# Kernel tuning notes

Hardware: AMD Instinct MI355X
Metric: run time of the kernel (lower is better)

## Reference

```python
import jax, jax.numpy as jnp
import numpy as np

B, G, C = 8, 512, 32  # batch, grid size, channel width (INIT_DIM)
NPB = 32768           # nonzeros per batch element


def _sconv(x, k, stride, pad):
    # dense conv; sparse semantics recovered by masking with the output
    # coordinate occupancy (Minkowski conv only produces active outputs)
    return jax.lax.conv_general_dilated(
        x, k, (stride, stride), [(pad, pad), (pad, pad)],
        dimension_numbers=('NHWC', 'HWIO', 'NHWC'))


def _downsample_mask(m):
    # ME strided output coord exists iff any input coord in the 2x2 cell is active
    return jax.lax.reduce_window(m, 0.0, jax.lax.max, (1, 2, 2, 1), (1, 2, 2, 1), 'VALID')


def setup_inputs() -> dict:
    key = jax.random.key(0)
    ks = jax.random.split(key, 16)
    b = jnp.repeat(jnp.arange(B, dtype=jnp.int32), NPB)
    yx = jax.random.randint(ks[0], (B * NPB, 2), 0, G, dtype=jnp.int32)
    coords = jnp.concatenate([b[:, None], yx], axis=1)          # [N,3] (b,y,x)
    feats = jax.random.normal(ks[1], (B * NPB, 1), jnp.float32)  # 1 feature/nnz
    x2 = jax.random.normal(ks[2], (B, 3), jnp.float32)
    # Minkowski conv kernels (bias=False by default); HWIO layout
    K1 = jax.random.normal(ks[3], (5, 5, 1, C), jnp.float32) * 0.28   # kaiming-ish
    K2 = jax.random.normal(ks[4], (3, 3, C, C), jnp.float32) * 0.083
    K3 = jax.random.normal(ks[5], (3, 3, C, C), jnp.float32) * 0.083
    K4 = jax.random.normal(ks[6], (3, 3, C, C), jnp.float32) * 0.083
    # feature MLP: Linear(3,64) -> ReLU -> Linear(64,32)
    W1 = jax.random.normal(ks[7], (3, 64), jnp.float32) * 0.3
    b1 = jnp.zeros((64,), jnp.float32)
    W2 = jax.random.normal(ks[8], (64, 32), jnp.float32) * 0.25
    b2 = jnp.zeros((32,), jnp.float32)
    # matrix_embedding: Linear(64,128) -> ReLU
    W3 = jax.random.normal(ks[9], (64, 128), jnp.float32) * 0.18
    b3 = jnp.zeros((128,), jnp.float32)
    return {'coords': coords, 'feats': feats, 'x2': x2,
            'K1': K1, 'K2': K2, 'K3': K3, 'K4': K4,
            'W1': W1, 'b1': b1, 'W2': W2, 'b2': b2, 'W3': W3, 'b3': b3}


def reference(coords, feats, x2, K1, K2, K3, K4, W1, b1, W2, b2, W3, b3):
    bi, yi, xi = coords[:, 0], coords[:, 1], coords[:, 2]
    grid = jnp.zeros((B, G, G, 1), jnp.float32).at[bi, yi, xi, 0].set(feats[:, 0])
    m1 = jnp.zeros((B, G, G, 1), jnp.float32).at[bi, yi, xi, 0].set(1.0)
    # layer1: k=5 s=1 (output coords == input coords)
    y1 = jax.nn.relu(_sconv(grid, K1, 1, 2)) * m1
    # layers 2-4: k=3 s=2; centered at even positions, masked by strided occupancy
    m2 = _downsample_mask(m1)
    y2 = jax.nn.relu(_sconv(y1, K2, 2, 1)) * m2
    m3 = _downsample_mask(m2)
    y3 = jax.nn.relu(_sconv(y2, K3, 2, 1)) * m3
    m4 = _downsample_mask(m3)
    y4 = jax.nn.relu(_sconv(y3, K4, 2, 1)) * m4
    # global average pool over active output coordinates per batch
    cnt = jnp.sum(m4, axis=(1, 2))                      # [B,1]
    pooled = jnp.sum(y4, axis=(1, 2)) / jnp.maximum(cnt, 1.0)  # [B,32]
    # aux feature MLP
    h = jax.nn.relu(x2[:, :3] @ W1 + b1) @ W2 + b2      # [B,32]
    z = jnp.concatenate([pooled, h], axis=1)            # [B,64]
    return jax.nn.relu(z @ W3 + b3)                     # [B,128]
```

## Files before the change

kernel.cpp:

```cpp
#include <hip/hip_runtime.h>
#include <hip/hip_bf16.h>
#include <stdint.h>


static constexpr int G_ = 512;
static constexpr int NPTS = 8 * 32768;

#define DEVI __device__ __forceinline__

typedef __attribute__((ext_vector_type(8))) short bf16x8;
typedef __attribute__((ext_vector_type(4))) float f32x4;
typedef __attribute__((ext_vector_type(4))) unsigned u32x4;

DEVI float bf_lo(unsigned w) { return __uint_as_float(w << 16); }
DEVI float bf_hi(unsigned w) { return __uint_as_float(w & 0xFFFF0000u); }
DEVI unsigned comp(const uint4& v, int i) {
  return i == 0 ? v.x : i == 1 ? v.y : i == 2 ? v.z : v.w;
}
DEVI unsigned short f2bf_bits(float f) {
  unsigned u = __float_as_uint(f);
  unsigned r = u + 0x7FFFu + ((u >> 16) & 1u);
  return (unsigned short)(r >> 16);
}
DEVI unsigned pack2(float a, float b) {
  return (unsigned)f2bf_bits(a) | ((unsigned)f2bf_bits(b) << 16);
}

__global__ __launch_bounds__(256) void k_scatter(const int* __restrict__ coords,
                                                 int* __restrict__ idxg) {
  int i = blockIdx.x * 256 + threadIdx.x;
  if (i >= NPTS) return;
  int b = coords[3 * i], y = coords[3 * i + 1], x = coords[3 * i + 2];
  atomicMax(&idxg[((size_t)b * G_ + y) * G_ + x], i);
}

__global__ __launch_bounds__(256) void k_grid(const int* __restrict__ idxg,
                                              const float* __restrict__ feats,
                                              unsigned* __restrict__ grid2) {
  int i = blockIdx.x * 256 + threadIdx.x;
  int v = idxg[i];
  float f = (v >= 0) ? feats[v] : 0.0f;
  unsigned short hb = f2bf_bits(f);
  unsigned short lb = f2bf_bits(f - __uint_as_float((unsigned)hb << 16));
  grid2[i] = (unsigned)hb | ((unsigned)lb << 16);
}

__global__ __launch_bounds__(256) void k_packw(
    const float* __restrict__ K1f, const float* __restrict__ K2,
    const float* __restrict__ K3, const float* __restrict__ K4,
    unsigned short* __restrict__ pw1h, unsigned short* __restrict__ pw1l,
    unsigned short* __restrict__ pw2, unsigned short* __restrict__ pw3,
    unsigned short* __restrict__ pw4) {
  const int t = threadIdx.x;
  if (t < 128) {
    int h = t >> 6, ln = t & 63;
    int g2 = ln >> 4, co = 2 * (ln & 15) + h;
#pragma unroll
    for (int j = 0; j < 8; j++) {
      int k = 8 * g2 + j;
      float v = (k < 25) ? K1f[k * 32 + co] : 0.f;
      unsigned short hb = f2bf_bits(v);
      pw1h[t * 8 + j] = hb;
      pw1l[t * 8 + j] = f2bf_bits(v - __uint_as_float((unsigned)hb << 16));
    }
  }
  const float* Ks[3] = {K2, K3, K4};
  unsigned short* ps[3] = {pw2, pw3, pw4};
  for (int m = 0; m < 3; m++)
    for (int e = t; e < 1152; e += 256) {
      int kk = e >> 7, rem = e & 127;
      int h = rem >> 6, ln = rem & 63;
      int g2 = ln >> 4, co = 2 * (ln & 15) + h;
#pragma unroll
      for (int j = 0; j < 8; j++)
        ps[m][e * 8 + j] = f2bf_bits(Ks[m][((kk * 32) + 8 * g2 + j) * 32 + co]);
    }
}

__global__ __launch_bounds__(256) void k_masks(const int* __restrict__ idxg,
                                               float* __restrict__ m2,
                                               float* __restrict__ m3,
                                               float* __restrict__ m4) {
  __shared__ float sm2[32][32];
  __shared__ float sm3[16][16];
  const int b = blockIdx.z, ty0 = blockIdx.y * 32, tx0 = blockIdx.x * 32;
  const int t = threadIdx.x;
  for (int i = t; i < 1024; i += 256) {
    int r = i >> 5, c = i & 31;
    const int* p = idxg + ((size_t)b * 512 + 2 * (ty0 + r)) * 512 + 2 * (tx0 + c);
    float v = ((p[0] & p[1] & p[512] & p[513]) >= 0) ? 1.f : 0.f;
    m2[((size_t)b * 256 + ty0 + r) * 256 + tx0 + c] = v;
    sm2[r][c] = v;
  }
  __syncthreads();
  {
    int r = t >> 4, c = t & 15;
    float v = fmaxf(fmaxf(sm2[2 * r][2 * c], sm2[2 * r][2 * c + 1]),
                    fmaxf(sm2[2 * r + 1][2 * c], sm2[2 * r + 1][2 * c + 1]));
    m3[((size_t)b * 128 + (ty0 >> 1) + r) * 128 + (tx0 >> 1) + c] = v;
    sm3[r][c] = v;
  }
  __syncthreads();
  if (t < 64) {
    int r = t >> 3, c = t & 7;
    float v = fmaxf(fmaxf(sm3[2 * r][2 * c], sm3[2 * r][2 * c + 1]),
                    fmaxf(sm3[2 * r + 1][2 * c], sm3[2 * r + 1][2 * c + 1]));
    m4[((size_t)b * 64 + (ty0 >> 2) + r) * 64 + (tx0 >> 2) + c] = v;
  }
}

__global__ __launch_bounds__(256, 3) void k_conv12(
    const unsigned* __restrict__ grid2, const int* __restrict__ idxg,
    const unsigned short* __restrict__ pw1h,
    const unsigned short* __restrict__ pw1l,
    const unsigned short* __restrict__ pw2, const float* __restrict__ m2,
    __hip_bfloat16* __restrict__ y2) {
  __shared__ unsigned s_grid[21 * 40];
  __shared__ unsigned short s_m1[17 * 34];
  __shared__ unsigned short s_y1[17 * 33 * 32];

  const int t = threadIdx.x;
  const int b = blockIdx.z, by = blockIdx.y, bx = blockIdx.x;
  const int gyb = 16 * by - 3, gxb = 32 * bx - 3;
  const size_t ibase = (size_t)b * G_ * G_;

  for (int i = t; i < 21 * 37; i += 256) {
    int rr = i / 37, cc = i - rr * 37;
    int gy = gyb + rr, gx = gxb + cc;
    unsigned v = 0;
    if (gy >= 0 && gy < G_ && gx >= 0 && gx < G_)
      v = grid2[ibase + (size_t)gy * G_ + gx];
    s_grid[rr * 40 + cc] = v;
  }
  for (int i = t; i < 17 * 33; i += 256) {
    int rr = i / 33, cc = i - rr * 33;
    int gy = gyb + 2 + rr, gx = gxb + 2 + cc;
    unsigned short mv = 0;
    if (gy >= 0 && gy < G_ && gx >= 0 && gx < G_)
      mv = (idxg[ibase + (size_t)gy * G_ + gx] >= 0) ? 1 : 0;
    s_m1[rr * 34 + cc] = mv;
  }

  const int lane = t & 63, w = t >> 6;
  const int r = lane & 15, g = lane >> 4;

  bf16x8 b1h[2], b1l[2];
#pragma unroll
  for (int h = 0; h < 2; h++) {
    b1h[h] = *(const bf16x8*)&pw1h[(h * 64 + lane) * 8];
    b1l[h] = *(const bf16x8*)&pw1l[(h * 64 + lane) * 8];
  }
  bf16x8 bw2[9][2];
#pragma unroll
  for (int kk = 0; kk < 9; kk++)
#pragma unroll
    for (int h = 0; h < 2; h++)
      bw2[kk][h] = *(const bf16x8*)&pw2[((kk * 2 + h) * 64 + lane) * 8];

  int reloff[8]; bool tval[8];
#pragma unroll
  for (int j = 0; j < 8; j++) {
    int k = 8 * g + j;
    tval[j] = (k < 25);
    int kq = tval[j] ? k : 0;
    reloff[j] = (kq / 5) * 40 + (kq % 5);
  }

  __syncthreads();

  for (int seg = w; seg < 36; seg += 4) {
    int piy, pix;
    if (seg < 34) { piy = seg >> 1; pix = ((seg & 1) << 4) + r; }
    else          { piy = (seg - 34) + r; pix = 32; }
    const int tapb = piy * 40 + pix;
    unsigned wv[8];
#pragma unroll
    for (int j = 0; j < 8; j++)
      wv[j] = tval[j] ? s_grid[tapb + reloff[j]] : 0u;
    u32x4 ua, ul;
#pragma unroll
    for (int p = 0; p < 4; p++) {
      unsigned w0 = wv[2 * p], w1 = wv[2 * p + 1];
      ua[p] = (w0 & 0xffffu) | (w1 << 16);
      ul[p] = (w0 >> 16) | (w1 & 0xffff0000u);
    }
    bf16x8 ahv = __builtin_bit_cast(bf16x8, ua);
    bf16x8 alv = __builtin_bit_cast(bf16x8, ul);
    f32x4 acc0 = {0.f, 0.f, 0.f, 0.f}, acc1 = {0.f, 0.f, 0.f, 0.f};
    acc0 = __builtin_amdgcn_mfma_f32_16x16x32_bf16(ahv, b1h[0], acc0, 0, 0, 0);
    acc1 = __builtin_amdgcn_mfma_f32_16x16x32_bf16(ahv, b1h[1], acc1, 0, 0, 0);
    acc0 = __builtin_amdgcn_mfma_f32_16x16x32_bf16(ahv, b1l[0], acc0, 0, 0, 0);
    acc1 = __builtin_amdgcn_mfma_f32_16x16x32_bf16(ahv, b1l[1], acc1, 0, 0, 0);
    acc0 = __builtin_amdgcn_mfma_f32_16x16x32_bf16(alv, b1h[0], acc0, 0, 0, 0);
    acc1 = __builtin_amdgcn_mfma_f32_16x16x32_bf16(alv, b1h[1], acc1, 0, 0, 0);
#pragma unroll
    for (int q = 0; q < 4; q++) {
      const int m = g * 4 + q;
      int eiy, eix;
      if (seg < 34) { eiy = seg >> 1; eix = ((seg & 1) << 4) + m; }
      else          { eiy = (seg - 34) + m; eix = 32; }
      float mk = (float)s_m1[eiy * 34 + eix];
      unsigned ov = pack2(fmaxf(acc0[q], 0.f) * mk, fmaxf(acc1[q], 0.f) * mk);
      int slot = eiy * 33 + eix;
      unsigned byo = (unsigned)(slot * 64 + 4 * r) ^
                     ((((unsigned)slot >> 1) & 7u) << 4);
      *(unsigned*)((char*)s_y1 + byo) = ov;
    }
  }
  __syncthreads();

  const int ty0 = 8 * by, tx0 = 16 * bx;
  for (int oy = w; oy < 8; oy += 4) {
    f32x4 acc0 = {0.f, 0.f, 0.f, 0.f}, acc1 = {0.f, 0.f, 0.f, 0.f};
#pragma unroll
    for (int ky = 0; ky < 3; ky++) {
      const int iy = 2 * oy + ky;
#pragma unroll
      for (int kx = 0; kx < 3; kx++) {
        const int slot = iy * 33 + 2 * r + kx;
        unsigned byo = (unsigned)(slot * 64 + g * 16) ^
                       ((((unsigned)slot >> 1) & 7u) << 4);
        bf16x8 a = *(const bf16x8*)((char*)s_y1 + byo);
        acc0 = __builtin_amdgcn_mfma_f32_16x16x32_bf16(a, bw2[ky * 3 + kx][0],
                                                       acc0, 0, 0, 0);
        acc1 = __builtin_amdgcn_mfma_f32_16x16x32_bf16(a, bw2[ky * 3 + kx][1],
                                                       acc1, 0, 0, 0);
      }
    }
    const size_t rowo = ((size_t)b * 256 + ty0 + oy) * 256;
#pragma unroll
    for (int q = 0; q < 4; q++) {
      const int m = g * 4 + q;
      const size_t opix = rowo + tx0 + m;
      const float mk = m2[opix];
      unsigned ov = pack2(fmaxf(acc0[q], 0.f) * mk, fmaxf(acc1[q], 0.f) * mk);
      *(unsigned*)(y2 + opix * 32 + 2 * r) = ov;
    }
  }
}

template <int HI, int SEGS, int NW>
__global__ __launch_bounds__(NW * 64) void k_conv3x3s2_mfma(
    const __hip_bfloat16* __restrict__ in,
    const unsigned short* __restrict__ pw,
    const float* __restrict__ mask, __hip_bfloat16* __restrict__ out) {
  constexpr int WI = HI, HO = HI / 2, WO = WI / 2;
  constexpr int NSEG = WO / 16 / SEGS;
  const int t = threadIdx.x;
  const int lane = t & 63, w = t >> 6;
  const int r = lane & 15, g = lane >> 4;
  bf16x8 bw[9][2];
#pragma unroll
  for (int kk = 0; kk < 9; kk++)
#pragma unroll
    for (int h = 0; h < 2; h++)
      bw[kk][h] = *(const bf16x8*)&pw[((kk * 2 + h) * 64 + lane) * 8];

  const int b = blockIdx.z;
  const int oy = blockIdx.y * NW + w;
  const int ox_base = blockIdx.x * (WO / SEGS);
  const __hip_bfloat16* inb = in + (size_t)b * HI * WI * 32;

  for (int s = 0; s < NSEG; s++) {
    const int ox0 = ox_base + s * 16;
    f32x4 acc0 = {0.f, 0.f, 0.f, 0.f}, acc1 = {0.f, 0.f, 0.f, 0.f};
#pragma unroll
    for (int ky = 0; ky < 3; ky++) {
      const int iy = 2 * oy + ky - 1;
      const __hip_bfloat16* rowp = inb + (size_t)(iy < 0 ? 0 : iy) * WI * 32;
#pragma unroll
      for (int kx = 0; kx < 3; kx++) {
        const int ix = 2 * (ox0 + r) + kx - 1;
        uint4 v = *(const uint4*)(rowp + (size_t)(ix < 0 ? 0 : ix) * 32 + g * 8);
        if ((iy | ix) < 0) { v.x = 0; v.y = 0; v.z = 0; v.w = 0; }
        bf16x8 a = *reinterpret_cast<const bf16x8*>(&v);
        acc0 = __builtin_amdgcn_mfma_f32_16x16x32_bf16(a, bw[ky * 3 + kx][0],
                                                       acc0, 0, 0, 0);
        acc1 = __builtin_amdgcn_mfma_f32_16x16x32_bf16(a, bw[ky * 3 + kx][1],
                                                       acc1, 0, 0, 0);
      }
    }
    const size_t rowo = ((size_t)b * HO + oy) * WO;
#pragma unroll
    for (int q = 0; q < 4; q++) {
      const size_t opix = rowo + (ox0 + g * 4 + q);
      const float m = mask[opix];
      unsigned ov = pack2(fmaxf(acc0[q], 0.f) * m, fmaxf(acc1[q], 0.f) * m);
      *(unsigned*)(out + opix * 32 + 2 * r) = ov;
    }
  }
}

__global__ __launch_bounds__(256) void k_pool(const __hip_bfloat16* __restrict__ y4,
                                              const float* __restrict__ m4,
                                              float* __restrict__ pooled) {
  const int b = blockIdx.x, t = threadIdx.x;
  const int c8 = t & 3, g = t >> 2;
  float s[8] = {0, 0, 0, 0, 0, 0, 0, 0};
  for (int p = g; p < 4096; p += 64) {
    uint4 raw = *(const uint4*)(y4 + ((size_t)b * 4096 + p) * 32 + c8 * 8);
#pragma unroll
    for (int cp = 0; cp < 4; cp++) {
      unsigned w = comp(raw, cp);
      s[2 * cp] += bf_lo(w);
      s[2 * cp + 1] += bf_hi(w);
    }
  }
  __shared__ float s_red[64][32];
  __shared__ float s_cnt[256];
#pragma unroll
  for (int j = 0; j < 8; j++) s_red[g][c8 * 8 + j] = s[j];
  float cnt = 0;
  for (int p = t; p < 4096; p += 256) cnt += m4[(size_t)b * 4096 + p];
  s_cnt[t] = cnt;
  __syncthreads();
  for (int st = 32; st > 0; st >>= 1) {
    if (g < st) {
#pragma unroll
      for (int j = 0; j < 8; j++) s_red[g][c8 * 8 + j] += s_red[g + st][c8 * 8 + j];
    }
    __syncthreads();
  }
  for (int st = 128; st > 0; st >>= 1) {
    if (t < st) s_cnt[t] += s_cnt[t + st];
    __syncthreads();
  }
  if (t < 32) pooled[b * 32 + t] = s_red[0][t] / fmaxf(s_cnt[0], 1.f);
}

__global__ __launch_bounds__(256) void k_mlp(
    const float* __restrict__ pooled, const float* __restrict__ x2,
    const float* __restrict__ W1, const float* __restrict__ b1,
    const float* __restrict__ W2, const float* __restrict__ b2,
    const float* __restrict__ W3, const float* __restrict__ b3,
    float* __restrict__ outp) {
  __shared__ float s_h1[8 * 64];
  __shared__ float s_z[8 * 64];
  const int t = threadIdx.x;
  for (int i = t; i < 512; i += 256) {
    int bb = i >> 6, j = i & 63;
    float a = b1[j] + x2[bb * 3 + 0] * W1[0 * 64 + j] +
              x2[bb * 3 + 1] * W1[1 * 64 + j] + x2[bb * 3 + 2] * W1[2 * 64 + j];
    s_h1[i] = fmaxf(a, 0.f);
  }
  __syncthreads();
  {
    int bb = t >> 5, ci = t & 31;
    float a = b2[ci];
    for (int k = 0; k < 64; k++) a += s_h1[bb * 64 + k] * W2[k * 32 + ci];
    s_z[bb * 64 + 32 + ci] = a;
    s_z[bb * 64 + ci] = pooled[bb * 32 + ci];
  }
  __syncthreads();
  for (int o = t; o < 1024; o += 256) {
    int bb = o >> 7, j = o & 127;
    float a = b3[j];
    for (int k = 0; k < 64; k++) a += s_z[bb * 64 + k] * W3[k * 128 + j];
    outp[o] = fmaxf(a, 0.f);
  }
}

extern "C" void kernel_launch(void* const* d_in, const int* in_sizes, int n_in,
                              void* d_out, int out_size, void* d_ws,
                              size_t ws_size, hipStream_t stream) {
  const int* coords = (const int*)d_in[0];
  const float* feats = (const float*)d_in[1];
  const float* x2 = (const float*)d_in[2];
  const float* K1 = (const float*)d_in[3];
  const float* K2 = (const float*)d_in[4];
  const float* K3 = (const float*)d_in[5];
  const float* K4 = (const float*)d_in[6];
  const float* W1 = (const float*)d_in[7];
  const float* b1 = (const float*)d_in[8];
  const float* W2 = (const float*)d_in[9];
  const float* b2 = (const float*)d_in[10];
  const float* W3 = (const float*)d_in[11];
  const float* b3 = (const float*)d_in[12];
  float* outp = (float*)d_out;

  char* ws = (char*)d_ws;
  size_t off = 0;
  auto alloc = [&](size_t bytes) {
    char* p = ws + off;
    off += (bytes + 255) & ~(size_t)255;
    return p;
  };
  int* idxg = (int*)alloc(8ull * 512 * 512 * 4);
  unsigned* grid2 = (unsigned*)alloc(8ull * 512 * 512 * 4);
  __hip_bfloat16* y2 = (__hip_bfloat16*)alloc(8ull * 256 * 256 * 32 * 2);
  __hip_bfloat16* y3 = (__hip_bfloat16*)alloc(8ull * 128 * 128 * 32 * 2);
  __hip_bfloat16* y4 = (__hip_bfloat16*)alloc(8ull * 64 * 64 * 32 * 2);
  float* m2 = (float*)alloc(8ull * 256 * 256 * 4);
  float* m3 = (float*)alloc(8ull * 128 * 128 * 4);
  float* m4 = (float*)alloc(8ull * 64 * 64 * 4);
  float* pooled = (float*)alloc(8 * 32 * 4);
  unsigned short* pw1h = (unsigned short*)alloc(128 * 8 * 2);
  unsigned short* pw1l = (unsigned short*)alloc(128 * 8 * 2);
  unsigned short* pw2 = (unsigned short*)alloc(1152 * 8 * 2);
  unsigned short* pw3 = (unsigned short*)alloc(1152 * 8 * 2);
  unsigned short* pw4 = (unsigned short*)alloc(1152 * 8 * 2);
  (void)ws_size; (void)in_sizes; (void)n_in; (void)out_size;

  hipMemsetAsync(idxg, 0xFF, 8ull * 512 * 512 * 4, stream);

  k_packw<<<1, 256, 0, stream>>>(K1, K2, K3, K4, pw1h, pw1l, pw2, pw3, pw4);
  k_scatter<<<NPTS / 256, 256, 0, stream>>>(coords, idxg);
  k_grid<<<(8 * 512 * 512) / 256, 256, 0, stream>>>(idxg, feats, grid2);
  k_masks<<<dim3(8, 8, 8), 256, 0, stream>>>(idxg, m2, m3, m4);

  k_conv12<<<dim3(16, 32, 8), 256, 0, stream>>>(grid2, idxg, pw1h, pw1l, pw2,
                                                m2, y2);

  k_conv3x3s2_mfma<256, 2, 4><<<dim3(2, 32, 8), 256, 0, stream>>>(y2, pw3, m3, y3);
  k_conv3x3s2_mfma<128, 4, 1><<<dim3(4, 64, 8), 64, 0, stream>>>(y3, pw4, m4, y4);

  k_pool<<<8, 256, 0, stream>>>(y4, m4, pooled);
  k_mlp<<<1, 256, 0, stream>>>(pooled, x2, W1, b1, W2, b2, W3, b3, outp);
}
```

Measured before the change: 226.8 us.

## Swap MFMA operands for vectorized epilogue stores and fold weight packing into mask kernel

The MFMA operand order is swapped so each lane holds 8 contiguous output channels of one pixel. Weights are repacked with a matching channel permutation, which lets the epilogues write 16-byte uint4 stores and apply the occupancy mask as a bitwise AND instead of a float multiply. The separate single-block weight-packing kernel is merged into block 0 of the mask kernel to save a launch. The layer-3 conv launch geometry is also changed (more blocks, fewer warps each), and the layer-2 weight register loads are deferred until after the layer-1 phase to lower register pressure.

```diff
diff --git a/kernel.cpp b/kernel.cpp
--- a/kernel.cpp
+++ b/kernel.cpp
@@ -10,7 +10,6 @@
 
 typedef __attribute__((ext_vector_type(8))) short bf16x8;
 typedef __attribute__((ext_vector_type(4))) float f32x4;
-typedef __attribute__((ext_vector_type(4))) unsigned u32x4;
 
 DEVI float bf_lo(unsigned w) { return __uint_as_float(w << 16); }
 DEVI float bf_hi(unsigned w) { return __uint_as_float(w & 0xFFFF0000u); }
@@ -22,8 +21,16 @@
   unsigned r = u + 0x7FFFu + ((u >> 16) & 1u);
   return (unsigned short)(r >> 16);
 }
-DEVI unsigned pack2(float a, float b) {
+DEVI unsigned pkbf(float a, float b) {
   return (unsigned)f2bf_bits(a) | ((unsigned)f2bf_bits(b) << 16);
+}
+DEVI uint4 quad_pack(const f32x4& a0, const f32x4& a1, unsigned msk) {
+  uint4 o;
+  o.x = pkbf(fmaxf(a0[0], 0.f), fmaxf(a0[1], 0.f)) & msk;
+  o.y = pkbf(fmaxf(a0[2], 0.f), fmaxf(a0[3], 0.f)) & msk;
+  o.z = pkbf(fmaxf(a1[0], 0.f), fmaxf(a1[1], 0.f)) & msk;
+  o.w = pkbf(fmaxf(a1[2], 0.f), fmaxf(a1[3], 0.f)) & msk;
+  return o;
 }
 
 __global__ __launch_bounds__(256) void k_scatter(const int* __restrict__ coords,
@@ -45,46 +52,48 @@
   grid2[i] = (unsigned)hb | ((unsigned)lb << 16);
 }
 
-__global__ __launch_bounds__(256) void k_packw(
+__global__ __launch_bounds__(256) void k_masks(
+    const int* __restrict__ idxg, float* __restrict__ m2,
+    float* __restrict__ m3, float* __restrict__ m4,
     const float* __restrict__ K1f, const float* __restrict__ K2,
     const float* __restrict__ K3, const float* __restrict__ K4,
     unsigned short* __restrict__ pw1h, unsigned short* __restrict__ pw1l,
     unsigned short* __restrict__ pw2, unsigned short* __restrict__ pw3,
     unsigned short* __restrict__ pw4) {
-  const int t = threadIdx.x;
-  if (t < 128) {
-    int h = t >> 6, ln = t & 63;
-    int g2 = ln >> 4, co = 2 * (ln & 15) + h;
-#pragma unroll
-    for (int j = 0; j < 8; j++) {
-      int k = 8 * g2 + j;
-      float v = (k < 25) ? K1f[k * 32 + co] : 0.f;
-      unsigned short hb = f2bf_bits(v);
-      pw1h[t * 8 + j] = hb;
-      pw1l[t * 8 + j] = f2bf_bits(v - __uint_as_float((unsigned)hb << 16));
-    }
-  }
-  const float* Ks[3] = {K2, K3, K4};
-  unsigned short* ps[3] = {pw2, pw3, pw4};
-  for (int m = 0; m < 3; m++)
-    for (int e = t; e < 1152; e += 256) {
-      int kk = e >> 7, rem = e & 127;
-      int h = rem >> 6, ln = rem & 63;
-      int g2 = ln >> 4, co = 2 * (ln & 15) + h;
-#pragma unroll
-      for (int j = 0; j < 8; j++)
-        ps[m][e * 8 + j] = f2bf_bits(Ks[m][((kk * 32) + 8 * g2 + j) * 32 + co]);
-    }
-}
-
-__global__ __launch_bounds__(256) void k_masks(const int* __restrict__ idxg,
-                                               float* __restrict__ m2,
-                                               float* __restrict__ m3,
-                                               float* __restrict__ m4) {
   __shared__ float sm2[32][32];
   __shared__ float sm3[16][16];
   const int b = blockIdx.z, ty0 = blockIdx.y * 32, tx0 = blockIdx.x * 32;
   const int t = threadIdx.x;
+
+  if (blockIdx.x == 0 && blockIdx.y == 0 && blockIdx.z == 0) {
+    if (t < 128) {
+      int h = t >> 6, ln = t & 63;
+      int m = ln & 15, g2 = ln >> 4;
+      int co = 8 * (m >> 2) + (m & 3) + 4 * h;
+#pragma unroll
+      for (int j = 0; j < 8; j++) {
+        int k = 8 * g2 + j;
+        float v = (k < 25) ? K1f[k * 32 + co] : 0.f;
+        unsigned short hb = f2bf_bits(v);
+        pw1h[t * 8 + j] = hb;
+        pw1l[t * 8 + j] = f2bf_bits(v - __uint_as_float((unsigned)hb << 16));
+      }
+    }
+    const float* Ks[3] = {K2, K3, K4};
+    unsigned short* ps[3] = {pw2, pw3, pw4};
+    for (int m_ = 0; m_ < 3; m_++)
+      for (int e = t; e < 1152; e += 256) {
+        int kk = e >> 7, rem = e & 127;
+        int h = rem >> 6, ln = rem & 63;
+        int m = ln & 15, g2 = ln >> 4;
+        int co = 8 * (m >> 2) + (m & 3) + 4 * h;
+#pragma unroll
+        for (int j = 0; j < 8; j++)
+          ps[m_][e * 8 + j] =
+              f2bf_bits(Ks[m_][((kk * 32) + 8 * g2 + j) * 32 + co]);
+      }
+  }
+
   for (int i = t; i < 1024; i += 256) {
     int r = i >> 5, c = i & 31;
     const int* p = idxg + ((size_t)b * 512 + 2 * (ty0 + r)) * 512 + 2 * (tx0 + c);
@@ -150,12 +159,6 @@
     b1h[h] = *(const bf16x8*)&pw1h[(h * 64 + lane) * 8];
     b1l[h] = *(const bf16x8*)&pw1l[(h * 64 + lane) * 8];
   }
-  bf16x8 bw2[9][2];
-#pragma unroll
-  for (int kk = 0; kk < 9; kk++)
-#pragma unroll
-    for (int h = 0; h < 2; h++)
-      bw2[kk][h] = *(const bf16x8*)&pw2[((kk * 2 + h) * 64 + lane) * 8];
 
   int reloff[8]; bool tval[8];
 #pragma unroll
@@ -169,47 +172,53 @@
   __syncthreads();
 
   for (int seg = w; seg < 36; seg += 4) {
-    int piy, pix;
-    if (seg < 34) { piy = seg >> 1; pix = ((seg & 1) << 4) + r; }
-    else          { piy = (seg - 34) + r; pix = 32; }
-    const int tapb = piy * 40 + pix;
+    int eiy, eix;
+    if (seg < 34) { eiy = seg >> 1; eix = ((seg & 1) << 4) + r; }
+    else          { eiy = (seg - 34) + r; eix = 32; }
+    const int tapb = eiy * 40 + eix;
     unsigned wv[8];
 #pragma unroll
     for (int j = 0; j < 8; j++)
       wv[j] = tval[j] ? s_grid[tapb + reloff[j]] : 0u;
-    u32x4 ua, ul;
+    uint4 ua, ul;
 #pragma unroll
     for (int p = 0; p < 4; p++) {
-      unsigned w0 = wv[2 * p], w1 = wv[2 * p + 1];
-      ua[p] = (w0 & 0xffffu) | (w1 << 16);
-      ul[p] = (w0 >> 16) | (w1 & 0xffff0000u);
-    }
-    bf16x8 ahv = __builtin_bit_cast(bf16x8, ua);
-    bf16x8 alv = __builtin_bit_cast(bf16x8, ul);
+      unsigned lo = __builtin_amdgcn_perm(wv[2 * p + 1], wv[2 * p], 0x05040100u);
+      unsigned hi = __builtin_amdgcn_perm(wv[2 * p + 1], wv[2 * p], 0x07060302u);
+      if (p == 0) { ua.x = lo; ul.x = hi; }
+      else if (p == 1) { ua.y = lo; ul.y = hi; }
+      else if (p == 2) { ua.z = lo; ul.z = hi; }
+      else { ua.w = lo; ul.w = hi; }
+    }
+    bf16x8 ph = __builtin_bit_cast(bf16x8, ua);
+    bf16x8 pl = __builtin_bit_cast(bf16x8, ul);
     f32x4 acc0 = {0.f, 0.f, 0.f, 0.f}, acc1 = {0.f, 0.f, 0.f, 0.f};
-    acc0 = __builtin_amdgcn_mfma_f32_16x16x32_bf16(ahv, b1h[0], acc0, 0, 0, 0);
-    acc1 = __builtin_amdgcn_mfma_f32_16x16x32_bf16(ahv, b1h[1], acc1, 0, 0, 0);
-    acc0 = __builtin_amdgcn_mfma_f32_16x16x32_bf16(ahv, b1l[0], acc0, 0, 0, 0);
-    acc1 = __builtin_amdgcn_mfma_f32_16x16x32_bf16(ahv, b1l[1], acc1, 0, 0, 0);
-    acc0 = __builtin_amdgcn_mfma_f32_16x16x32_bf16(alv, b1h[0], acc0, 0, 0, 0);
-    acc1 = __builtin_amdgcn_mfma_f32_16x16x32_bf16(alv, b1h[1], acc1, 0, 0, 0);
-#pragma unroll
-    for (int q = 0; q < 4; q++) {
-      const int m = g * 4 + q;
-      int eiy, eix;
-      if (seg < 34) { eiy = seg >> 1; eix = ((seg & 1) << 4) + m; }
-      else          { eiy = (seg - 34) + m; eix = 32; }
-      float mk = (float)s_m1[eiy * 34 + eix];
-      unsigned ov = pack2(fmaxf(acc0[q], 0.f) * mk, fmaxf(acc1[q], 0.f) * mk);
-      int slot = eiy * 33 + eix;
-      unsigned byo = (unsigned)(slot * 64 + 4 * r) ^
-                     ((((unsigned)slot >> 1) & 7u) << 4);
-      *(unsigned*)((char*)s_y1 + byo) = ov;
-    }
-  }
+    acc0 = __builtin_amdgcn_mfma_f32_16x16x32_bf16(b1h[0], ph, acc0, 0, 0, 0);
+    acc1 = __builtin_amdgcn_mfma_f32_16x16x32_bf16(b1h[1], ph, acc1, 0, 0, 0);
+    acc0 = __builtin_amdgcn_mfma_f32_16x16x32_bf16(b1l[0], ph, acc0, 0, 0, 0);
+    acc1 = __builtin_amdgcn_mfma_f32_16x16x32_bf16(b1l[1], ph, acc1, 0, 0, 0);
+    acc0 = __builtin_amdgcn_mfma_f32_16x16x32_bf16(b1h[0], pl, acc0, 0, 0, 0);
+    acc1 = __builtin_amdgcn_mfma_f32_16x16x32_bf16(b1h[1], pl, acc1, 0, 0, 0);
+
+    unsigned msk = s_m1[eiy * 34 + eix] ? 0xFFFFFFFFu : 0u;
+    uint4 o = quad_pack(acc0, acc1, msk);
+    int slot = eiy * 33 + eix;
+    unsigned byo = (unsigned)(slot * 64 + 16 * g) ^
+                   ((((unsigned)slot >> 1) & 7u) << 4);
+    *(uint4*)((char*)s_y1 + byo) = o;
+  }
+
+  bf16x8 bw2[9][2];
+#pragma unroll
+  for (int kk = 0; kk < 9; kk++)
+#pragma unroll
+    for (int h = 0; h < 2; h++)
+      bw2[kk][h] = *(const bf16x8*)&pw2[((kk * 2 + h) * 64 + lane) * 8];
+
   __syncthreads();
 
   const int ty0 = 8 * by, tx0 = 16 * bx;
+  const unsigned* m2u = (const unsigned*)m2;
   for (int oy = w; oy < 8; oy += 4) {
     f32x4 acc0 = {0.f, 0.f, 0.f, 0.f}, acc1 = {0.f, 0.f, 0.f, 0.f};
 #pragma unroll
@@ -221,21 +230,16 @@
         unsigned byo = (unsigned)(slot * 64 + g * 16) ^
                        ((((unsigned)slot >> 1) & 7u) << 4);
         bf16x8 a = *(const bf16x8*)((char*)s_y1 + byo);
-        acc0 = __builtin_amdgcn_mfma_f32_16x16x32_bf16(a, bw2[ky * 3 + kx][0],
+        acc0 = __builtin_amdgcn_mfma_f32_16x16x32_bf16(bw2[ky * 3 + kx][0], a,
                                                        acc0, 0, 0, 0);
-        acc1 = __builtin_amdgcn_mfma_f32_16x16x32_bf16(a, bw2[ky * 3 + kx][1],
+        acc1 = __builtin_amdgcn_mfma_f32_16x16x32_bf16(bw2[ky * 3 + kx][1], a,
                                                        acc1, 0, 0, 0);
       }
     }
-    const size_t rowo = ((size_t)b * 256 + ty0 + oy) * 256;
-#pragma unroll
-    for (int q = 0; q < 4; q++) {
-      const int m = g * 4 + q;
-      const size_t opix = rowo + tx0 + m;
-      const float mk = m2[opix];
-      unsigned ov = pack2(fmaxf(acc0[q], 0.f) * mk, fmaxf(acc1[q], 0.f) * mk);
-      *(unsigned*)(y2 + opix * 32 + 2 * r) = ov;
-    }
+    const size_t opix = ((size_t)b * 256 + ty0 + oy) * 256 + tx0 + r;
+    unsigned msk = m2u[opix] ? 0xFFFFFFFFu : 0u;
+    uint4 o = quad_pack(acc0, acc1, msk);
+    *(uint4*)(y2 + opix * 32 + 8 * g) = o;
   }
 }
 
@@ -260,6 +264,7 @@
   const int oy = blockIdx.y * NW + w;
   const int ox_base = blockIdx.x * (WO / SEGS);
   const __hip_bfloat16* inb = in + (size_t)b * HI * WI * 32;
+  const unsigned* masku = (const unsigned*)mask;
 
   for (int s = 0; s < NSEG; s++) {
     const int ox0 = ox_base + s * 16;
@@ -274,20 +279,16 @@
         uint4 v = *(const uint4*)(rowp + (size_t)(ix < 0 ? 0 : ix) * 32 + g * 8);
         if ((iy | ix) < 0) { v.x = 0; v.y = 0; v.z = 0; v.w = 0; }
         bf16x8 a = *reinterpret_cast<const bf16x8*>(&v);
-        acc0 = __builtin_amdgcn_mfma_f32_16x16x32_bf16(a, bw[ky * 3 + kx][0],
+        acc0 = __builtin_amdgcn_mfma_f32_16x16x32_bf16(bw[ky * 3 + kx][0], a,
                                                        acc0, 0, 0, 0);
-        acc1 = __builtin_amdgcn_mfma_f32_16x16x32_bf16(a, bw[ky * 3 + kx][1],
+        acc1 = __builtin_amdgcn_mfma_f32_16x16x32_bf16(bw[ky * 3 + kx][1], a,
                                                        acc1, 0, 0, 0);
       }
     }
-    const size_t rowo = ((size_t)b * HO + oy) * WO;
-#pragma unroll
-    for (int q = 0; q < 4; q++) {
-      const size_t opix = rowo + (ox0 + g * 4 + q);
-      const float m = mask[opix];
-      unsigned ov = pack2(fmaxf(acc0[q], 0.f) * m, fmaxf(acc1[q], 0.f) * m);
-      *(unsigned*)(out + opix * 32 + 2 * r) = ov;
-    }
+    const size_t opix = ((size_t)b * HO + oy) * WO + ox0 + r;
+    unsigned msk = masku[opix] ? 0xFFFFFFFFu : 0u;
+    uint4 o = quad_pack(acc0, acc1, msk);
+    *(uint4*)(out + opix * 32 + 8 * g) = o;
   }
 }
 
@@ -401,17 +402,17 @@
   unsigned short* pw4 = (unsigned short*)alloc(1152 * 8 * 2);
   (void)ws_size; (void)in_sizes; (void)n_in; (void)out_size;
 
-  hipMemsetAsync(idxg, 0xFF, 8ull * 512 * 512 * 4, stream);
-
-  k_packw<<<1, 256, 0, stream>>>(K1, K2, K3, K4, pw1h, pw1l, pw2, pw3, pw4);
+  (void)hipMemsetAsync(idxg, 0xFF, 8ull * 512 * 512 * 4, stream);
+
   k_scatter<<<NPTS / 256, 256, 0, stream>>>(coords, idxg);
   k_grid<<<(8 * 512 * 512) / 256, 256, 0, stream>>>(idxg, feats, grid2);
-  k_masks<<<dim3(8, 8, 8), 256, 0, stream>>>(idxg, m2, m3, m4);
+  k_masks<<<dim3(8, 8, 8), 256, 0, stream>>>(idxg, m2, m3, m4, K1, K2, K3, K4,
+                                             pw1h, pw1l, pw2, pw3, pw4);
 
   k_conv12<<<dim3(16, 32, 8), 256, 0, stream>>>(grid2, idxg, pw1h, pw1l, pw2,
                                                 m2, y2);
 
-  k_conv3x3s2_mfma<256, 2, 4><<<dim3(2, 32, 8), 256, 0, stream>>>(y2, pw3, m3, y3);
+  k_conv3x3s2_mfma<256, 4, 2><<<dim3(4, 64, 8), 128, 0, stream>>>(y2, pw3, m3, y3);
   k_conv3x3s2_mfma<128, 4, 1><<<dim3(4, 64, 8), 64, 0, stream>>>(y3, pw4, m4, y4);
 
   k_pool<<<8, 256, 0, stream>>>(y4, m4, pooled);
```

New measurement: 206.9 us. -8.8%, faster.
